# Performance work log

Measured on AMD Instinct MI355X. Metric: run time of the kernel, lower is better.

The kernel has to match this reference:

```python
import jax, jax.numpy as jnp
import numpy as np
import math

N_MENTIONS = 8192
EMB = 1024


def setup_inputs() -> dict:
    key = jax.random.key(0)
    k0, k1, k2 = jax.random.split(key, 3)
    scale = 1.0 / math.sqrt(EMB)
    return {
        "all_mentions": jax.random.normal(k0, (N_MENTIONS, EMB), dtype=jnp.float32),
        "Wq": jax.random.normal(k1, (EMB, EMB), dtype=jnp.float32) * scale,
        "bq": jnp.zeros((EMB,), dtype=jnp.float32),
        "Wk": jax.random.normal(k2, (EMB, EMB), dtype=jnp.float32) * scale,
        "bk": jnp.zeros((EMB,), dtype=jnp.float32),
    }


def reference(all_mentions, Wq, bq, Wk, bk):
    # torch.nn.Linear: y = x @ W.T + b
    E = all_mentions.shape[-1]
    q = (all_mentions @ Wq.T + bq) / jnp.sqrt(jnp.asarray(E, all_mentions.dtype))
    k = all_mentions @ Wk.T + bk
    # [N, N] raw attention logits
    attn = q @ k.T
    # causal mask: -inf strictly above the diagonal (triu, diagonal=1)
    n = all_mentions.shape[0]
    mask = jnp.where(jnp.triu(jnp.ones((n, n), dtype=bool), k=1),
                     jnp.asarray(-jnp.inf, attn.dtype),
                     jnp.asarray(0.0, attn.dtype))
    # Module returns attn_weights = masked pre-softmax logits (single layer,
    # single head, bsz=1); the softmax@v branch is discarded by the caller.
    return attn + mask
```

## Files before the change

### kernel.cpp

```cpp
#include <hip/hip_runtime.h>
#include <math.h>

#define NM 8192
#define KDIM 1024

#define NEG_BIG (-3.0e38f)

typedef __attribute__((ext_vector_type(4))) float floatx4;
typedef __attribute__((ext_vector_type(8))) _Float16 halfx8;
typedef __attribute__((ext_vector_type(4))) _Float16 halfx4;

__device__ __forceinline__ void gload_lds16(const void* g, void* l) {
    __builtin_amdgcn_global_load_lds(
        (const __attribute__((address_space(1))) void*)g,
        (__attribute__((address_space(3))) void*)l,
        16, 0, 0);
}

__global__ __launch_bounds__(256)
void convert_kernel(const float* __restrict__ X,
                    const float* __restrict__ Wq,
                    const float* __restrict__ Wk,
                    _Float16* __restrict__ Xf,
                    _Float16* __restrict__ Wqf,
                    _Float16* __restrict__ Wkf) {
    const int XB = (NM * KDIM) / 4 / 256;
    const int WB = (KDIM * KDIM) / 4 / 256;
    int b = blockIdx.x;
    const float* src;
    _Float16* dst;
    if (b < XB)            { src = X;  dst = Xf; }
    else if (b < XB + WB)  { b -= XB;       src = Wq; dst = Wqf; }
    else                   { b -= XB + WB;  src = Wk; dst = Wkf; }
    const int i = b * 256 + threadIdx.x;
    floatx4 v = ((const floatx4*)src)[i];
    halfx4 h;
    h.x = (_Float16)v.x;
    h.y = (_Float16)v.y;
    h.z = (_Float16)v.z;
    h.w = (_Float16)v.w;
    *(halfx4*)&dst[(size_t)i * 4] = h;
}


#define GEMM_PIPE_BODY(APTR, BPTR)                                            \
    auto STAGE = [&](int kt, int pb) {                                        \
        const int k0 = kt * 32;                                               \
        _Pragma("unroll")                                                     \
        for (int c = 0; c < 4; c++) {               \
            const int r = c * 64 + srow;                                      \
            gload_lds16(APTR + (size_t)(row0 + r) * KDIM + k0 + skoff,        \
                        &sA[pb][(c * 256 + t) * 8]);                          \
        }                                                                     \
        _Pragma("unroll")                                                     \
        for (int c = 0; c < 2; c++) {               \
            const int r = c * 64 + srow;                                      \
            gload_lds16(BPTR + (size_t)(col0 + r) * KDIM + k0 + skoff,        \
                        &sB[pb][(c * 256 + t) * 8]);                          \
        }                                                                     \
    };                                                                        \
    STAGE(0, 0);                                                              \
    STAGE(1, 1);                                                              \
    asm volatile("s_waitcnt vmcnt(6)" ::: "memory");       \
    __builtin_amdgcn_s_barrier();                                             \
    for (int kt = 0; kt < 32; ++kt) {                                         \
        const int pb = kt & 1;                                                \
        halfx8 a[8], b[4];                                                    \
        _Pragma("unroll")                                                     \
        for (int i = 0; i < 8; i++) {                                         \
            const int r = wr + i * 16 + l15;                                  \
            a[i] = *(const halfx8*)&sA[pb][r * 32 + fsl];                     \
        }                                                                     \
        _Pragma("unroll")                                                     \
        for (int j = 0; j < 4; j++) {                                         \
            const int r = wc + j * 16 + l15;                                  \
            b[j] = *(const halfx8*)&sB[pb][r * 32 + fsl];                     \
        }                                                                     \
        asm volatile("s_waitcnt lgkmcnt(0)" ::: "memory");                    \
        __builtin_amdgcn_sched_barrier(0);                                    \
        __builtin_amdgcn_s_barrier();                                         \
        if (kt < 30) STAGE(kt + 2, pb);                                       \
        __builtin_amdgcn_s_setprio(1);                                        \
        _Pragma("unroll")                                                     \
        for (int j = 0; j < 4; j++)                                           \
            _Pragma("unroll")                                                 \
            for (int i = 0; i < 8; i++)                                       \
                acc[i][j] = __builtin_amdgcn_mfma_f32_16x16x32_f16(           \
                    a[i], b[j], acc[i][j], 0, 0, 0);                          \
        __builtin_amdgcn_s_setprio(0);                                        \
        if (kt < 30)                                                          \
            asm volatile("s_waitcnt vmcnt(6)" ::: "memory");                  \
        else if (kt == 30)                                                    \
            asm volatile("s_waitcnt vmcnt(0)" ::: "memory");                  \
        if (kt < 31) __builtin_amdgcn_s_barrier();                            \
    }

__global__ __launch_bounds__(256, 2)
void proj_kernel(const _Float16* __restrict__ Xf,
                 const _Float16* __restrict__ Wqf, const float* __restrict__ bq,
                 _Float16* __restrict__ Qf,
                 const _Float16* __restrict__ Wkf, const float* __restrict__ bk,
                 _Float16* __restrict__ Kf) {
    const bool isK = (blockIdx.z == 1);
    const _Float16* W    = isK ? Wkf : Wqf;
    const float*    bias = isK ? bk : bq;
    _Float16*       O    = isK ? Kf : Qf;
    const float scale = isK ? 1.0f : 0.03125f;

    __shared__ __attribute__((aligned(16))) _Float16 sA[2][256 * 32];
    __shared__ __attribute__((aligned(16))) _Float16 sB[2][128 * 32];

    const int t = threadIdx.x;
    const int lane = t & 63;
    const int quad = lane >> 4;
    const int l15 = lane & 15;
    const int wave = t >> 6;
    const int wr = (wave & 1) * 128;
    const int wc = (wave >> 1) * 64;

    const int row0 = blockIdx.y * 256;
    const int col0 = blockIdx.x * 128;

    const int srow = t >> 2;
    const int skoff = (((t & 3) ^ ((t >> 3) & 3)) * 8);
    const int fsl = (quad ^ ((l15 >> 1) & 3)) * 8;

    floatx4 zero = {0.f, 0.f, 0.f, 0.f};
    floatx4 acc[8][4];
#pragma unroll
    for (int i = 0; i < 8; i++)
#pragma unroll
        for (int j = 0; j < 4; j++) acc[i][j] = zero;

    GEMM_PIPE_BODY(Xf, W)

#pragma unroll
    for (int i = 0; i < 8; i++)
#pragma unroll
        for (int j = 0; j < 4; j++)
#pragma unroll
            for (int r = 0; r < 4; r++) {
                const int grow = row0 + wr + i * 16 + quad * 4 + r;
                const int gcol = col0 + wc + j * 16 + l15;
                const float v = (acc[i][j][r] + bias[gcol]) * scale;
                O[(size_t)grow * KDIM + gcol] = (_Float16)v;
            }
}

__global__ __launch_bounds__(256, 2)
void attn_kernel(const _Float16* __restrict__ Qf,
                 const _Float16* __restrict__ Kf,
                 float* __restrict__ out) {
    const int lid = blockIdx.x;
    const int x = lid & 7;
    const int s = lid >> 3;
    const int bi = s & 31;
    const int bj = ((s >> 5) << 3) + x;
    const int t = threadIdx.x;

    if (bj * 128 > bi * 256 + 255) {
        const floatx4 v = {NEG_BIG, NEG_BIG, NEG_BIG, NEG_BIG};
        floatx4* o4 = (floatx4*)(out + (size_t)bi * 256 * NM + (size_t)bj * 128);
#pragma unroll
        for (int it = 0; it < 32; ++it) {
            const int idx = it * 256 + t;
            const int r = idx >> 5;
            const int c = idx & 31;
            __builtin_nontemporal_store(v, &o4[(size_t)r * (NM / 4) + c]);
        }
        return;
    }

    __shared__ __attribute__((aligned(16))) _Float16 sA[2][256 * 32];
    __shared__ __attribute__((aligned(16))) _Float16 sB[2][128 * 32];

    const int lane = t & 63;
    const int quad = lane >> 4;
    const int l15 = lane & 15;
    const int wave = t >> 6;
    const int wr = (wave & 1) * 128;
    const int wc = (wave >> 1) * 64;

    const int row0 = bi * 256;
    const int col0 = bj * 128;

    const int srow = t >> 2;
    const int skoff = (((t & 3) ^ ((t >> 3) & 3)) * 8);
    const int fsl = (quad ^ ((l15 >> 1) & 3)) * 8;

    floatx4 zero = {0.f, 0.f, 0.f, 0.f};
    floatx4 acc[8][4];
#pragma unroll
    for (int i = 0; i < 8; i++)
#pragma unroll
        for (int j = 0; j < 4; j++) acc[i][j] = zero;

    GEMM_PIPE_BODY(Qf, Kf)

#pragma unroll
    for (int i = 0; i < 8; i++)
#pragma unroll
        for (int j = 0; j < 4; j++)
#pragma unroll
            for (int r = 0; r < 4; r++) {
                const int grow = row0 + wr + i * 16 + quad * 4 + r;
                const int gcol = col0 + wc + j * 16 + l15;
                const float v = (gcol <= grow) ? acc[i][j][r] : NEG_BIG;
                __builtin_nontemporal_store(v, &out[(size_t)grow * NM + gcol]);
            }
}

extern "C" void kernel_launch(void* const* d_in, const int* in_sizes, int n_in,
                              void* d_out, int out_size, void* d_ws, size_t ws_size,
                              hipStream_t stream) {
    const float* X  = (const float*)d_in[0];
    const float* Wq = (const float*)d_in[1];
    const float* bq = (const float*)d_in[2];
    const float* Wk = (const float*)d_in[3];
    const float* bk = (const float*)d_in[4];
    float* out = (float*)d_out;

    _Float16* p = (_Float16*)d_ws;
    const size_t XN = (size_t)NM * KDIM;
    const size_t WN = (size_t)KDIM * KDIM;
    _Float16* Xf  = p;  p += XN;
    _Float16* Wqf = p;  p += WN;
    _Float16* Wkf = p;  p += WN;
    _Float16* Qf  = p;  p += XN;
    _Float16* Kf  = p;  p += XN;

    const int nconv = (int)((XN + 2 * WN) / 4 / 256);
    convert_kernel<<<nconv, 256, 0, stream>>>(X, Wq, Wk, Xf, Wqf, Wkf);

    dim3 pgrid(KDIM / 128, NM / 256, 2);
    proj_kernel<<<pgrid, 256, 0, stream>>>(Xf, Wqf, bq, Qf, Wkf, bk, Kf);

    attn_kernel<<<(NM / 256) * (NM / 128), 256, 0, stream>>>(Qf, Kf, out);
}
```

Before: 419.7 us.

## Restructure GEMM pipeline to 512 threads, K=64 tiles, triple-buffered dynamic LDS

Both GEMM kernels move from 256 to 512 threads per block, with each of 8 waves computing a 64x64 subtile. The K tile is enlarged to 64 with a three-deep LDS ring in dynamic shared memory. Global-to-LDS loads for stage kt+2 are split into two halves, each interleaved with one of the two MFMA sub-steps, and a new XOR swizzle is used. The goal is better latency hiding and fewer barriers per K element. The cost is about 147KB of LDS per block, which likely limits residency to one block per CU.

```diff
diff --git a/kernel.cpp b/kernel.cpp
--- a/kernel.cpp
+++ b/kernel.cpp
@@ -9,6 +9,8 @@
 typedef __attribute__((ext_vector_type(4))) float floatx4;
 typedef __attribute__((ext_vector_type(8))) _Float16 halfx8;
 typedef __attribute__((ext_vector_type(4))) _Float16 halfx4;
+
+#define SMEM_BYTES (3 * (256 * 64 + 128 * 64) * 2)
 
 __device__ __forceinline__ void gload_lds16(const void* g, void* l) {
     __builtin_amdgcn_global_load_lds(
@@ -44,58 +46,103 @@
 
 
 #define GEMM_PIPE_BODY(APTR, BPTR)                                            \
-    auto STAGE = [&](int kt, int pb) {                                        \
-        const int k0 = kt * 32;                                               \
-        _Pragma("unroll")                                                     \
-        for (int c = 0; c < 4; c++) {               \
-            const int r = c * 64 + srow;                                      \
-            gload_lds16(APTR + (size_t)(row0 + r) * KDIM + k0 + skoff,        \
-                        &sA[pb][(c * 256 + t) * 8]);                          \
-        }                                                                     \
-        _Pragma("unroll")                                                     \
-        for (int c = 0; c < 2; c++) {               \
-            const int r = c * 64 + srow;                                      \
-            gload_lds16(BPTR + (size_t)(col0 + r) * KDIM + k0 + skoff,        \
-                        &sB[pb][(c * 256 + t) * 8]);                          \
-        }                                                                     \
+    extern __shared__ _Float16 smem[];                                        \
+    _Float16* const sAl = smem;                           \
+    _Float16* const sBl = smem + 3 * 16384;               \
+    const int t = threadIdx.x;                                                \
+    const int lane = t & 63;                                                  \
+    const int quad = lane >> 4;                                               \
+    const int l15 = lane & 15;                                                \
+    const int wv = t >> 6;                                                    \
+    const int wr = (wv >> 1) * 64;                \
+    const int wc = (wv & 1) * 64;                 \
+    const int srow = t >> 3;             \
+    const int skoff = ((t & 7) ^ ((t >> 3) & 7)) * 8;     \
+    auto stA = [&](int kt, int pb, int c) {                                   \
+        gload_lds16(APTR + (size_t)(row0 + c * 64 + srow) * KDIM              \
+                         + kt * 64 + skoff,                                   \
+                    sAl + pb * 16384 + (c * 512 + t) * 8);                    \
     };                                                                        \
-    STAGE(0, 0);                                                              \
-    STAGE(1, 1);                                                              \
+    auto stB = [&](int kt, int pb, int c) {                                   \
+        gload_lds16(BPTR + (size_t)(col0 + c * 64 + srow) * KDIM              \
+                         + kt * 64 + skoff,                                   \
+                    sBl + pb * 8192 + (c * 512 + t) * 8);                     \
+    };                                                                        \
+    floatx4 acc[4][4];                                                        \
+    _Pragma("unroll")                                                         \
+    for (int i = 0; i < 4; i++)                                               \
+        _Pragma("unroll")                                                     \
+        for (int j = 0; j < 4; j++) acc[i][j] = (floatx4){0.f, 0.f, 0.f, 0.f}; \
+    stA(0, 0, 0); stA(0, 0, 1); stA(0, 0, 2); stA(0, 0, 3);                   \
+    stB(0, 0, 0); stB(0, 0, 1);                                               \
+    stA(1, 1, 0); stA(1, 1, 1); stA(1, 1, 2); stA(1, 1, 3);                   \
+    stB(1, 1, 0); stB(1, 1, 1);                                               \
     asm volatile("s_waitcnt vmcnt(6)" ::: "memory");       \
     __builtin_amdgcn_s_barrier();                                             \
-    for (int kt = 0; kt < 32; ++kt) {                                         \
-        const int pb = kt & 1;                                                \
-        halfx8 a[8], b[4];                                                    \
-        _Pragma("unroll")                                                     \
-        for (int i = 0; i < 8; i++) {                                         \
+    _Pragma("unroll")                                                         \
+    for (int kt = 0; kt < 16; ++kt) {                                         \
+        const int pb = kt % 3;                                                \
+        const int pq = (kt + 2) % 3;                                          \
+        halfx8 a[4], b[4];                                                    \
+                                              \
+        if (kt < 14) { stA(kt + 2, pq, 0); stA(kt + 2, pq, 1);                \
+                       stB(kt + 2, pq, 0); }                                  \
+        _Pragma("unroll")                                                     \
+        for (int i = 0; i < 4; i++) {                                         \
             const int r = wr + i * 16 + l15;                                  \
-            a[i] = *(const halfx8*)&sA[pb][r * 32 + fsl];                     \
+            a[i] = *(const halfx8*)&sAl[pb * 16384 + r * 64 +                 \
+                                        ((quad ^ (r & 7)) * 8)];              \
         }                                                                     \
         _Pragma("unroll")                                                     \
         for (int j = 0; j < 4; j++) {                                         \
             const int r = wc + j * 16 + l15;                                  \
-            b[j] = *(const halfx8*)&sB[pb][r * 32 + fsl];                     \
-        }                                                                     \
+            b[j] = *(const halfx8*)&sBl[pb * 8192 + r * 64 +                  \
+                                        ((quad ^ (r & 7)) * 8)];              \
+        }                                                                     \
+        __builtin_amdgcn_s_barrier();                                         \
         asm volatile("s_waitcnt lgkmcnt(0)" ::: "memory");                    \
         __builtin_amdgcn_sched_barrier(0);                                    \
-        __builtin_amdgcn_s_barrier();                                         \
-        if (kt < 30) STAGE(kt + 2, pb);                                       \
         __builtin_amdgcn_s_setprio(1);                                        \
         _Pragma("unroll")                                                     \
         for (int j = 0; j < 4; j++)                                           \
             _Pragma("unroll")                                                 \
-            for (int i = 0; i < 8; i++)                                       \
+            for (int i = 0; i < 4; i++)                                       \
                 acc[i][j] = __builtin_amdgcn_mfma_f32_16x16x32_f16(           \
                     a[i], b[j], acc[i][j], 0, 0, 0);                          \
         __builtin_amdgcn_s_setprio(0);                                        \
-        if (kt < 30)                                                          \
-            asm volatile("s_waitcnt vmcnt(6)" ::: "memory");                  \
-        else if (kt == 30)                                                    \
-            asm volatile("s_waitcnt vmcnt(0)" ::: "memory");                  \
-        if (kt < 31) __builtin_amdgcn_s_barrier();                            \
+        __builtin_amdgcn_s_barrier();                                         \
+                                              \
+        if (kt < 14) { stA(kt + 2, pq, 2); stA(kt + 2, pq, 3);                \
+                       stB(kt + 2, pq, 1); }                                  \
+        _Pragma("unroll")                                                     \
+        for (int i = 0; i < 4; i++) {                                         \
+            const int r = wr + i * 16 + l15;                                  \
+            a[i] = *(const halfx8*)&sAl[pb * 16384 + r * 64 +                 \
+                                        (((4 + quad) ^ (r & 7)) * 8)];        \
+        }                                                                     \
+        _Pragma("unroll")                                                     \
+        for (int j = 0; j < 4; j++) {                                         \
+            const int r = wc + j * 16 + l15;                                  \
+            b[j] = *(const halfx8*)&sBl[pb * 8192 + r * 64 +                  \
+                                        (((4 + quad) ^ (r & 7)) * 8)];        \
+        }                                                                     \
+        __builtin_amdgcn_s_barrier();                                         \
+        asm volatile("s_waitcnt lgkmcnt(0)" ::: "memory");                    \
+        __builtin_amdgcn_sched_barrier(0);                                    \
+        __builtin_amdgcn_s_setprio(1);                                        \
+        _Pragma("unroll")                                                     \
+        for (int j = 0; j < 4; j++)                                           \
+            _Pragma("unroll")                                                 \
+            for (int i = 0; i < 4; i++)                                       \
+                acc[i][j] = __builtin_amdgcn_mfma_f32_16x16x32_f16(           \
+                    a[i], b[j], acc[i][j], 0, 0, 0);                          \
+        __builtin_amdgcn_s_setprio(0);                                        \
+        if (kt < 14)       asm volatile("s_waitcnt vmcnt(6)" ::: "memory");   \
+        else if (kt == 14) asm volatile("s_waitcnt vmcnt(0)" ::: "memory");   \
+        if (kt < 15) __builtin_amdgcn_s_barrier();                            \
     }
 
-__global__ __launch_bounds__(256, 2)
+__global__ __launch_bounds__(512, 2)
 void proj_kernel(const _Float16* __restrict__ Xf,
                  const _Float16* __restrict__ Wqf, const float* __restrict__ bq,
                  _Float16* __restrict__ Qf,
@@ -107,35 +154,13 @@
     _Float16*       O    = isK ? Kf : Qf;
     const float scale = isK ? 1.0f : 0.03125f;
 
-    __shared__ __attribute__((aligned(16))) _Float16 sA[2][256 * 32];
-    __shared__ __attribute__((aligned(16))) _Float16 sB[2][128 * 32];
-
-    const int t = threadIdx.x;
-    const int lane = t & 63;
-    const int quad = lane >> 4;
-    const int l15 = lane & 15;
-    const int wave = t >> 6;
-    const int wr = (wave & 1) * 128;
-    const int wc = (wave >> 1) * 64;
-
     const int row0 = blockIdx.y * 256;
     const int col0 = blockIdx.x * 128;
 
-    const int srow = t >> 2;
-    const int skoff = (((t & 3) ^ ((t >> 3) & 3)) * 8);
-    const int fsl = (quad ^ ((l15 >> 1) & 3)) * 8;
-
-    floatx4 zero = {0.f, 0.f, 0.f, 0.f};
-    floatx4 acc[8][4];
-#pragma unroll
-    for (int i = 0; i < 8; i++)
-#pragma unroll
-        for (int j = 0; j < 4; j++) acc[i][j] = zero;
-
     GEMM_PIPE_BODY(Xf, W)
 
 #pragma unroll
-    for (int i = 0; i < 8; i++)
+    for (int i = 0; i < 4; i++)
 #pragma unroll
         for (int j = 0; j < 4; j++)
 #pragma unroll
@@ -147,7 +172,7 @@
             }
 }
 
-__global__ __launch_bounds__(256, 2)
+__global__ __launch_bounds__(512, 2)
 void attn_kernel(const _Float16* __restrict__ Qf,
                  const _Float16* __restrict__ Kf,
                  float* __restrict__ out) {
@@ -156,14 +181,14 @@
     const int s = lid >> 3;
     const int bi = s & 31;
     const int bj = ((s >> 5) << 3) + x;
-    const int t = threadIdx.x;
 
     if (bj * 128 > bi * 256 + 255) {
+        const int tid = threadIdx.x;
         const floatx4 v = {NEG_BIG, NEG_BIG, NEG_BIG, NEG_BIG};
         floatx4* o4 = (floatx4*)(out + (size_t)bi * 256 * NM + (size_t)bj * 128);
 #pragma unroll
-        for (int it = 0; it < 32; ++it) {
-            const int idx = it * 256 + t;
+        for (int it = 0; it < 16; ++it) {
+            const int idx = it * 512 + tid;
             const int r = idx >> 5;
             const int c = idx & 31;
             __builtin_nontemporal_store(v, &o4[(size_t)r * (NM / 4) + c]);
@@ -171,34 +196,13 @@
         return;
     }
 
-    __shared__ __attribute__((aligned(16))) _Float16 sA[2][256 * 32];
-    __shared__ __attribute__((aligned(16))) _Float16 sB[2][128 * 32];
-
-    const int lane = t & 63;
-    const int quad = lane >> 4;
-    const int l15 = lane & 15;
-    const int wave = t >> 6;
-    const int wr = (wave & 1) * 128;
-    const int wc = (wave >> 1) * 64;
-
     const int row0 = bi * 256;
     const int col0 = bj * 128;
 
-    const int srow = t >> 2;
-    const int skoff = (((t & 3) ^ ((t >> 3) & 3)) * 8);
-    const int fsl = (quad ^ ((l15 >> 1) & 3)) * 8;
-
-    floatx4 zero = {0.f, 0.f, 0.f, 0.f};
-    floatx4 acc[8][4];
-#pragma unroll
-    for (int i = 0; i < 8; i++)
-#pragma unroll
-        for (int j = 0; j < 4; j++) acc[i][j] = zero;
-
     GEMM_PIPE_BODY(Qf, Kf)
 
 #pragma unroll
-    for (int i = 0; i < 8; i++)
+    for (int i = 0; i < 4; i++)
 #pragma unroll
         for (int j = 0; j < 4; j++)
 #pragma unroll
@@ -229,11 +233,20 @@
     _Float16* Qf  = p;  p += XN;
     _Float16* Kf  = p;  p += XN;
 
+    static bool attr_done = false;
+    if (!attr_done) {
+        hipFuncSetAttribute((const void*)proj_kernel,
+                            hipFuncAttributeMaxDynamicSharedMemorySize, SMEM_BYTES);
+        hipFuncSetAttribute((const void*)attn_kernel,
+                            hipFuncAttributeMaxDynamicSharedMemorySize, SMEM_BYTES);
+        attr_done = true;
+    }
+
     const int nconv = (int)((XN + 2 * WN) / 4 / 256);
     convert_kernel<<<nconv, 256, 0, stream>>>(X, Wq, Wk, Xf, Wqf, Wkf);
 
     dim3 pgrid(KDIM / 128, NM / 256, 2);
-    proj_kernel<<<pgrid, 256, 0, stream>>>(Xf, Wqf, bq, Qf, Wkf, bk, Kf);
-
-    attn_kernel<<<(NM / 256) * (NM / 128), 256, 0, stream>>>(Qf, Kf, out);
-}
+    proj_kernel<<<pgrid, 512, SMEM_BYTES, stream>>>(Xf, Wqf, bq, Qf, Wkf, bk, Kf);
+
+    attn_kernel<<<(NM / 256) * (NM / 128), 512, SMEM_BYTES, stream>>>(Qf, Kf, out);
+}
```

Result: slower. 434.4 us (+3.5%).
